# Kernel tuning notes

Measured on AMD Instinct MI355X. Metric: run time of the kernel, lower is better.

The kernel has to match this reference:

```python
import jax, jax.numpy as jnp
import numpy as np

HEADS = 4


def _dwconv(x, w, d):
    # x: (B,C,H,W), w: (C,1,3,3); reflection pad by d then dilated depthwise conv (same spatial size)
    xp = jnp.pad(x, ((0, 0), (0, 0), (d, d), (d, d)), mode='reflect')
    return jax.lax.conv_general_dilated(
        xp, w, window_strides=(1, 1), padding='VALID', rhs_dilation=(d, d),
        feature_group_count=x.shape[1], dimension_numbers=('NCHW', 'OIHW', 'NCHW'))


def _pyramid(x, w1, w2, w3):
    x0, x1, x2, x3 = jnp.split(x, 4, axis=1)
    return jnp.concatenate(
        [x0, _dwconv(x1, w1, 1), _dwconv(x2, w2, 2), _dwconv(x3, w3, 3)], axis=1)


def _conv1x1(x, w):
    return jnp.einsum('oi,bihw->bohw', w, x)


def _heads(t):
    # b (H c) h w -> b H c (h w)
    b, C, h, w = t.shape
    return t.reshape(b, HEADS, C // HEADS, h * w)


def _l2norm(t):
    # torch F.normalize(dim=-1): x / max(||x||, eps)
    return t / jnp.maximum(jnp.linalg.norm(t, axis=-1, keepdims=True), 1e-12)


def setup_inputs() -> dict:
    key = jax.random.key(0)
    ks = jax.random.split(key, 20)
    B, H, W = 2, 256, 256
    dim, dim_h, dim_l, sque = 256, 128, 64, 4
    s = 0.05
    inp = {
        'x':   jax.random.normal(ks[0], (B, dim, H, W), jnp.float32),
        'x_h': jax.random.normal(ks[1], (B, dim_h, H, W), jnp.float32),
        'x_l': jax.random.normal(ks[2], (B, dim_l, H, W), jnp.float32),
        # kv: 1x1 conv dim -> dim//sque*2 = 128, pyramid dw on 128 ch (32 per branch)
        'w_kv':  jax.random.normal(ks[3], (dim // sque * 2, dim), jnp.float32) * s,
        'kv_dw1': jax.random.normal(ks[4], (32, 1, 3, 3), jnp.float32) * s,
        'kv_dw2': jax.random.normal(ks[5], (32, 1, 3, 3), jnp.float32) * s,
        'kv_dw3': jax.random.normal(ks[6], (32, 1, 3, 3), jnp.float32) * s,
        # q_h: dim_h -> 32, pyramid branches of 8 ch
        'w_qh':  jax.random.normal(ks[7], (dim_h // sque, dim_h), jnp.float32) * s,
        'qh_dw1': jax.random.normal(ks[8], (8, 1, 3, 3), jnp.float32) * s,
        'qh_dw2': jax.random.normal(ks[9], (8, 1, 3, 3), jnp.float32) * s,
        'qh_dw3': jax.random.normal(ks[10], (8, 1, 3, 3), jnp.float32) * s,
        # q_l: dim_l -> 16, pyramid branches of 4 ch
        'w_ql':  jax.random.normal(ks[11], (dim_l // sque, dim_l), jnp.float32) * s,
        'ql_dw1': jax.random.normal(ks[12], (4, 1, 3, 3), jnp.float32) * s,
        'ql_dw2': jax.random.normal(ks[13], (4, 1, 3, 3), jnp.float32) * s,
        'ql_dw3': jax.random.normal(ks[14], (4, 1, 3, 3), jnp.float32) * s,
        'w_ph': jax.random.normal(ks[15], (dim_h, dim_h // sque), jnp.float32) * s,
        'w_pl': jax.random.normal(ks[16], (dim_l, dim_l // sque), jnp.float32) * s,
        'temperature': jnp.ones((HEADS, 1, 1), jnp.float32),
    }
    return inp


def reference(x, x_h, x_l, w_kv, kv_dw1, kv_dw2, kv_dw3,
              w_qh, qh_dw1, qh_dw2, qh_dw3,
              w_ql, ql_dw1, ql_dw2, ql_dw3,
              w_ph, w_pl, temperature):
    b, _, h, w = x.shape
    kv = _pyramid(_conv1x1(x, w_kv), kv_dw1, kv_dw2, kv_dw3)
    k, v = jnp.split(kv, 2, axis=1)
    q_h = _pyramid(_conv1x1(x_h, w_qh), qh_dw1, qh_dw2, qh_dw3)
    q_l = _pyramid(_conv1x1(x_l, w_ql), ql_dw1, ql_dw2, ql_dw3)
    k = _l2norm(_heads(k))      # (b, H, ck, N)
    v = _heads(v)               # (b, H, ck, N)
    q_h = _l2norm(_heads(q_h))  # (b, H, ch, N)
    q_l = _l2norm(_heads(q_l))  # (b, H, cl, N)
    temp = temperature[None]    # (1, H, 1, 1)

    def attend(q):
        a = jnp.einsum('bhcn,bhdn->bhcd', q, k) * temp  # channel-wise scores
        a = jax.nn.softmax(a, axis=-1)
        return jnp.einsum('bhcd,bhdn->bhcn', a, v)

    msg_h = attend(q_h).reshape(b, -1, h, w)
    msg_l = attend(q_l).reshape(b, -1, h, w)
    return _conv1x1(msg_h, w_ph), _conv1x1(msg_l, w_pl)
```

## Files before the change

### kernel.cpp

```cpp
#include <hip/hip_runtime.h>


#define NPIX 65536

using bf16x8 = __attribute__((ext_vector_type(8))) short;
using f32x4  = __attribute__((ext_vector_type(4))) float;

__device__ __forceinline__ unsigned short f2bf(float f) {
    unsigned u = __builtin_bit_cast(unsigned, f);
    u = u + 0x7FFF + ((u >> 16) & 1);
    return (unsigned short)(u >> 16);
}
__device__ __forceinline__ float bf2f(unsigned short u) {
    return __builtin_bit_cast(float, (unsigned)u << 16);
}

__global__ void zero_k(float* __restrict__ p, int n) {
    int i = blockIdx.x * 256 + threadIdx.x;
    if (i < n) p[i] = 0.f;
}

__global__ void cast_w_k(const float* __restrict__ w_kv,
                         const float* __restrict__ w_qh,
                         const float* __restrict__ w_ql,
                         unsigned short* __restrict__ wkv_b,
                         unsigned short* __restrict__ wqh_b,
                         unsigned short* __restrict__ wql_b) {
    int idx = blockIdx.x * 256 + threadIdx.x;
    if (idx < 32768) wkv_b[idx] = f2bf(w_kv[idx]);
    else if (idx < 32768 + 4096) wqh_b[idx - 32768] = f2bf(w_qh[idx - 32768]);
    else if (idx < 32768 + 4096 + 1024) wql_b[idx - 36864] = f2bf(w_ql[idx - 36864]);
}

template <int MW, int MSPLIT, int KT, bool SPLIT, bool SRCBF>
__global__ __launch_bounds__(256) void gemm_mfma_k(
    const void* __restrict__ srcv, const unsigned short* __restrict__ A,
    float* __restrict__ out, float* __restrict__ out2,
    long srcBStride, long aBStride, long outBStride, long out2BStride) {
    constexpr int K  = KT * 32;
    constexpr int RW = K / 2 + 4;
    constexpr int NW = MSPLIT;

    __shared__ unsigned Blds[64 * RW];

    const int t    = threadIdx.x;
    const int wave = t >> 6;
    const int lane = t & 63;
    const int r    = lane & 15;
    const int q    = lane >> 4;

    const int chunk = blockIdx.x;
    const int b     = chunk >> 10;
    const int n0    = (chunk & 1023) * 64;
    const int m0    = (wave % MSPLIT) * MW * 16;
    const int nb    = (wave / MSPLIT) * NW * 16;

    bf16x8 af[MW][KT];
    {
        const unsigned short* Ab = A + (size_t)b * aBStride;
#pragma unroll
        for (int mw = 0; mw < MW; ++mw)
#pragma unroll
            for (int kt = 0; kt < KT; ++kt)
                af[mw][kt] = *(const bf16x8*)(Ab + (size_t)(m0 + mw * 16 + r) * K + kt * 32 + q * 8);
    }

    {
        const int sn = t >> 2, kp0 = t & 3;
        if constexpr (SRCBF) {
            const unsigned short* sp = (const unsigned short*)srcv + (size_t)b * srcBStride + n0 + sn;
#pragma unroll
            for (int it = 0; it < K / 8; ++it) {
                const int kp = it * 4 + kp0;
                const unsigned v0 = sp[(size_t)(2 * kp) * NPIX];
                const unsigned v1 = sp[(size_t)(2 * kp + 1) * NPIX];
                Blds[sn * RW + kp] = v0 | (v1 << 16);
            }
        } else {
            const float* sp = (const float*)srcv + (size_t)b * srcBStride + n0 + sn;
#pragma unroll
            for (int it = 0; it < K / 8; ++it) {
                const int kp = it * 4 + kp0;
                const float v0 = sp[(size_t)(2 * kp) * NPIX];
                const float v1 = sp[(size_t)(2 * kp + 1) * NPIX];
                Blds[sn * RW + kp] = (unsigned)f2bf(v0) | ((unsigned)f2bf(v1) << 16);
            }
        }
    }
    __syncthreads();

    f32x4 acc[MW][NW];
#pragma unroll
    for (int mw = 0; mw < MW; ++mw)
#pragma unroll
        for (int nw = 0; nw < NW; ++nw) acc[mw][nw] = (f32x4){0.f, 0.f, 0.f, 0.f};

#pragma unroll
    for (int kt = 0; kt < KT; ++kt) {
        bf16x8 bf[NW];
#pragma unroll
        for (int nw = 0; nw < NW; ++nw) {
            const int n = nb + nw * 16 + r;
            bf[nw] = *(const bf16x8*)(&Blds[n * RW + kt * 16 + q * 4]);
        }
#pragma unroll
        for (int mw = 0; mw < MW; ++mw)
#pragma unroll
            for (int nw = 0; nw < NW; ++nw)
                acc[mw][nw] = __builtin_amdgcn_mfma_f32_16x16x32_bf16(
                    af[mw][kt], bf[nw], acc[mw][nw], 0, 0, 0);
    }

#pragma unroll
    for (int mw = 0; mw < MW; ++mw) {
        const int obase = m0 + mw * 16 + q * 4;
#pragma unroll
        for (int nw = 0; nw < NW; ++nw) {
            const int n = n0 + nb + nw * 16 + r;
#pragma unroll
            for (int rr = 0; rr < 4; ++rr) {
                const int o = obase + rr;
                float* dst;
                if (SPLIT && o >= 128)
                    dst = out2 + (size_t)b * out2BStride + (size_t)(o - 128) * NPIX + n;
                else
                    dst = out + (size_t)b * outBStride + (size_t)o * NPIX + n;
                *dst = acc[mw][nw][rr];
            }
        }
    }
}

__device__ __forceinline__ int refl(int p) {
    return (p < 0) ? -p : ((p > 255) ? 510 - p : p);
}

__global__ __launch_bounds__(256) void pyramid_k(const float* __restrict__ in,
                                                 unsigned short* __restrict__ out, int C,
                                                 const float* __restrict__ w1,
                                                 const float* __restrict__ w2,
                                                 const float* __restrict__ w3) {
    const int t = threadIdx.x;
    const int bi = blockIdx.x;
    const int y = bi & 255;
    const int bc = bi >> 8;
    const int G = C >> 2;
    const int c = bc % C;
    const int g = (c >= 3 * G) ? 3 : (c >= 2 * G) ? 2 : (c >= G) ? 1 : 0;

    const float* src = in + (size_t)bc * NPIX;
    const size_t oidx = (size_t)bc * NPIX + y * 256 + t;

    if (g == 0) {
        out[oidx] = f2bf(src[y * 256 + t]);
        return;
    }

    __shared__ float rows[3][256];
    const int y0 = refl(y - g), y2 = refl(y + g);
    for (int i = t; i < 384; i += 256) {
        const int rr  = i >> 7;
        const int off = (i & 127) * 2;
        const int yy  = (rr == 0) ? y0 : (rr == 1) ? y : y2;
        const float2 v = *(const float2*)(src + yy * 256 + off);
        rows[rr][off] = v.x;
        rows[rr][off + 1] = v.y;
    }
    __syncthreads();

    const float* wp = (g == 1 ? w1 : (g == 2 ? w2 : w3)) + (c - g * G) * 9;
    const int xm = refl(t - g), xp = refl(t + g);
    float s = 0.f;
#pragma unroll
    for (int ky = 0; ky < 3; ++ky) {
        s = fmaf(wp[ky * 3 + 0], rows[ky][xm], s);
        s = fmaf(wp[ky * 3 + 1], rows[ky][t], s);
        s = fmaf(wp[ky * 3 + 2], rows[ky][xp], s);
    }
    out[oidx] = f2bf(s);
}

__global__ __launch_bounds__(256) void scores_k(const unsigned short* __restrict__ qhp,
                                                const unsigned short* __restrict__ qlp,
                                                const unsigned short* __restrict__ kvp,
                                                float* __restrict__ Sbuf) {
    const int t = threadIdx.x;
    const int wave = t >> 6, lane = t & 63;
    const int r = lane & 15, q = lane >> 4;
    const int slice = blockIdx.x;
    const int hd = blockIdx.y;
    const int b = blockIdx.z;

    const unsigned short* qrow;
    if (r < 8)       qrow = qhp + (size_t)(b * 32 + hd * 8 + r) * NPIX;
    else if (r < 12) qrow = qlp + (size_t)(b * 16 + hd * 4 + (r - 8)) * NPIX;
    else             qrow = qhp + (size_t)(b * 32 + hd * 8) * NPIX;
    const unsigned short* krow = kvp + (size_t)(b * 128 + hd * 16 + r) * NPIX;

    const int base = slice * 1024 + wave * 256;
    f32x4 acc = (f32x4){0.f, 0.f, 0.f, 0.f};
    float qq = 0.f, kk = 0.f;
#pragma unroll
    for (int c8 = 0; c8 < 8; ++c8) {
        const int n = base + c8 * 32 + q * 8;
        const bf16x8 a  = *(const bf16x8*)(qrow + n);
        const bf16x8 bb = *(const bf16x8*)(krow + n);
        acc = __builtin_amdgcn_mfma_f32_16x16x32_bf16(a, bb, acc, 0, 0, 0);
#pragma unroll
        for (int j = 0; j < 8; ++j) {
            const float av = bf2f((unsigned short)a[j]);
            const float bv = bf2f((unsigned short)bb[j]);
            qq = fmaf(av, av, qq);
            kk = fmaf(bv, bv, kk);
        }
    }
    qq += __shfl_xor(qq, 16); qq += __shfl_xor(qq, 32);
    kk += __shfl_xor(kk, 16); kk += __shfl_xor(kk, 32);

    __shared__ float Sred[4][16][16];
    __shared__ float qred[4][16];
    __shared__ float kred[4][16];
#pragma unroll
    for (int rr = 0; rr < 4; ++rr) Sred[wave][q * 4 + rr][r] = acc[rr];
    if (q == 0) { qred[wave][r] = qq; kred[wave][r] = kk; }
    __syncthreads();

    if (t < 192) {
        const int c = t >> 4, d = t & 15;
        const float s = Sred[0][c][d] + Sred[1][c][d] + Sred[2][c][d] + Sred[3][c][d];
        if (c < 12) atomicAdd(&Sbuf[((b * 4 + hd) * 12 + c) * 16 + d], s);
    } else if (t < 208) {
        const int d = t - 192;
        const float s = kred[0][d] + kred[1][d] + kred[2][d] + kred[3][d];
        atomicAdd(&Sbuf[1536 + (b * 4 + hd) * 16 + d], s);
    } else if (t < 220) {
        const int c = t - 208;
        const float s = qred[0][c] + qred[1][c] + qred[2][c] + qred[3][c];
        atomicAdd(&Sbuf[1664 + (b * 4 + hd) * 12 + c], s);
    }
}

__global__ __launch_bounds__(256) void finalize_k(const float* __restrict__ Sbuf,
                                                  const float* __restrict__ w_ph,
                                                  const float* __restrict__ w_pl,
                                                  const float* __restrict__ temp,
                                                  unsigned short* __restrict__ CT) {
    __shared__ float As[192];
    const int t = threadIdx.x;
    const int hd = blockIdx.x;
    const int b = blockIdx.y;

    if (t < 192) {
        const int c = t >> 4, d = t & 15;
        const float kss = Sbuf[1536 + (b * 4 + hd) * 16 + d];
        const float qss = Sbuf[1664 + (b * 4 + hd) * 12 + c];
        const float invk = 1.f / fmaxf(sqrtf(kss), 1e-12f);
        const float invq = 1.f / fmaxf(sqrtf(qss), 1e-12f);
        float s = Sbuf[((b * 4 + hd) * 12 + c) * 16 + d] * invq * invk * temp[hd];
        float m = s;
        for (int mask = 8; mask >= 1; mask >>= 1) m = fmaxf(m, __shfl_xor(m, mask, 16));
        const float e = expf(s - m);
        float sum = e;
        for (int mask = 8; mask >= 1; mask >>= 1) sum += __shfl_xor(sum, mask, 16);
        As[c * 16 + d] = e / sum;
    }
    __syncthreads();

    unsigned short* CTb = CT + (size_t)b * 192 * 64;
    for (int idx = t; idx < 3072; idx += 256) {
        const int d = idx & 15, rr = idx >> 4;
        float s = 0.f;
        if (rr < 128) {
#pragma unroll
            for (int c = 0; c < 8; ++c)
                s = fmaf(w_ph[rr * 32 + hd * 8 + c], As[c * 16 + d], s);
        } else {
            const int r2 = rr - 128;
#pragma unroll
            for (int c = 0; c < 4; ++c)
                s = fmaf(w_pl[r2 * 16 + hd * 4 + c], As[(8 + c) * 16 + d], s);
        }
        CTb[(size_t)rr * 64 + hd * 16 + d] = f2bf(s);
    }
}

extern "C" void kernel_launch(void* const* d_in, const int* in_sizes, int n_in,
                              void* d_out, int out_size, void* d_ws, size_t ws_size,
                              hipStream_t stream) {
    const float* x      = (const float*)d_in[0];
    const float* x_h    = (const float*)d_in[1];
    const float* x_l    = (const float*)d_in[2];
    const float* w_kv   = (const float*)d_in[3];
    const float* kv_dw1 = (const float*)d_in[4];
    const float* kv_dw2 = (const float*)d_in[5];
    const float* kv_dw3 = (const float*)d_in[6];
    const float* w_qh   = (const float*)d_in[7];
    const float* qh_dw1 = (const float*)d_in[8];
    const float* qh_dw2 = (const float*)d_in[9];
    const float* qh_dw3 = (const float*)d_in[10];
    const float* w_ql   = (const float*)d_in[11];
    const float* ql_dw1 = (const float*)d_in[12];
    const float* ql_dw2 = (const float*)d_in[13];
    const float* ql_dw3 = (const float*)d_in[14];
    const float* w_ph   = (const float*)d_in[15];
    const float* w_pl   = (const float*)d_in[16];
    const float* temp   = (const float*)d_in[17];
    float* out = (float*)d_out;

    char* ws = (char*)d_ws;
    float*          Sbuf  = (float*)(ws + 0);
    unsigned short* wkv_b = (unsigned short*)(ws + 8192);
    unsigned short* wqh_b = (unsigned short*)(ws + 73728);
    unsigned short* wql_b = (unsigned short*)(ws + 81920);
    unsigned short* CT    = (unsigned short*)(ws + 90112);
    float*          kvraw = (float*)(ws + 262144);
    float*          qhraw = (float*)(ws + 67371008);
    float*          qlraw = (float*)(ws + 84148224);
    unsigned short* kvpyr = (unsigned short*)(ws + 92536832);
    unsigned short* qhpyr = (unsigned short*)(ws + 126091264);
    unsigned short* qlpyr = (unsigned short*)(ws + 134479872);

    zero_k<<<7, 256, 0, stream>>>(Sbuf, 1760);
    cast_w_k<<<148, 256, 0, stream>>>(w_kv, w_qh, w_ql, wkv_b, wqh_b, wql_b);

    gemm_mfma_k<2, 4, 8, false, false><<<2048, 256, 0, stream>>>(
        x, wkv_b, kvraw, nullptr, 256L * NPIX, 0L, 128L * NPIX, 0L);
    gemm_mfma_k<2, 1, 4, false, false><<<2048, 256, 0, stream>>>(
        x_h, wqh_b, qhraw, nullptr, 128L * NPIX, 0L, 32L * NPIX, 0L);
    gemm_mfma_k<1, 1, 2, false, false><<<2048, 256, 0, stream>>>(
        x_l, wql_b, qlraw, nullptr, 64L * NPIX, 0L, 16L * NPIX, 0L);

    pyramid_k<<<65536, 256, 0, stream>>>(kvraw, kvpyr, 128, kv_dw1, kv_dw2, kv_dw3);
    pyramid_k<<<16384, 256, 0, stream>>>(qhraw, qhpyr, 32, qh_dw1, qh_dw2, qh_dw3);
    pyramid_k<<<8192, 256, 0, stream>>>(qlraw, qlpyr, 16, ql_dw1, ql_dw2, ql_dw3);

    scores_k<<<dim3(64, 4, 2), 256, 0, stream>>>(qhpyr, qlpyr, kvpyr, Sbuf);
    finalize_k<<<dim3(4, 2), 256, 0, stream>>>(Sbuf, w_ph, w_pl, temp, CT);

    gemm_mfma_k<3, 4, 2, true, true><<<2048, 256, 0, stream>>>(
        (const void*)(kvpyr + 64L * NPIX), CT, out, out + 2L * 128 * NPIX,
        128L * NPIX, 192L * 64, 128L * NPIX, 64L * NPIX);
}
```

Before: 452.3 us.

## Pipeline GEMM chunks, fuse pyramid launches with row tiling, drop atomics

Each GEMM block now handles four pixel chunks, loading the next chunk from global memory into registers while computing the current one. It double-buffers an XOR-swizzled LDS tile and uses wide vector loads. The three pyramid launches become one kernel that processes 32-row tiles per plane with a shared halo, two pixels per thread and packed bf16 stores. Score reduction writes per-slice partials that finalize sums, replacing atomics and the zeroing kernel. The cost is more registers and LDS per block, fewer blocks in flight, and hand-placed waitcnt assembly that could be fragile.

```diff
diff --git a/kernel.cpp b/kernel.cpp
--- a/kernel.cpp
+++ b/kernel.cpp
@@ -5,6 +5,8 @@
 
 using bf16x8 = __attribute__((ext_vector_type(8))) short;
 using f32x4  = __attribute__((ext_vector_type(4))) float;
+using f4     = __attribute__((ext_vector_type(4))) float;
+using us4    = __attribute__((ext_vector_type(4))) unsigned short;
 
 __device__ __forceinline__ unsigned short f2bf(float f) {
     unsigned u = __builtin_bit_cast(unsigned, f);
@@ -13,11 +15,6 @@
 }
 __device__ __forceinline__ float bf2f(unsigned short u) {
     return __builtin_bit_cast(float, (unsigned)u << 16);
-}
-
-__global__ void zero_k(float* __restrict__ p, int n) {
-    int i = blockIdx.x * 256 + threadIdx.x;
-    if (i < n) p[i] = 0.f;
 }
 
 __global__ void cast_w_k(const float* __restrict__ w_kv,
@@ -32,28 +29,31 @@
     else if (idx < 32768 + 4096 + 1024) wql_b[idx - 36864] = f2bf(w_ql[idx - 36864]);
 }
 
-template <int MW, int MSPLIT, int KT, bool SPLIT, bool SRCBF>
-__global__ __launch_bounds__(256) void gemm_mfma_k(
+template <int MW, int MSPLIT, int KT, int CPB, bool SPLIT, bool SRCBF>
+__global__ __launch_bounds__(256, 2) void gemm_mfma_k(
     const void* __restrict__ srcv, const unsigned short* __restrict__ A,
     float* __restrict__ out, float* __restrict__ out2,
     long srcBStride, long aBStride, long outBStride, long out2BStride) {
-    constexpr int K  = KT * 32;
-    constexpr int RW = K / 2 + 4;
-    constexpr int NW = MSPLIT;
-
-    __shared__ unsigned Blds[64 * RW];
+    constexpr int K     = KT * 32;
+    constexpr int KW    = K / 2;
+    constexpr int NW    = MSPLIT;
+    constexpr int ITERS = K / 32;
+    constexpr int SCNT  = MW * NW * 4;
+
+    __shared__ __align__(16) unsigned Blds[2][64 * KW];
 
     const int t    = threadIdx.x;
     const int wave = t >> 6;
     const int lane = t & 63;
     const int r    = lane & 15;
     const int q    = lane >> 4;
-
-    const int chunk = blockIdx.x;
-    const int b     = chunk >> 10;
-    const int n0    = (chunk & 1023) * 64;
-    const int m0    = (wave % MSPLIT) * MW * 16;
-    const int nb    = (wave / MSPLIT) * NW * 16;
+    const int h    = t >> 4;
+    const int m4   = (t & 15) * 4;
+
+    const int chunk0 = blockIdx.x * CPB;
+    const int b      = chunk0 >> 10;
+    const int m0     = (wave % MSPLIT) * MW * 16;
+    const int nb     = (wave / MSPLIT) * NW * 16;
 
     bf16x8 af[MW][KT];
     {
@@ -65,68 +65,109 @@
                 af[mw][kt] = *(const bf16x8*)(Ab + (size_t)(m0 + mw * 16 + r) * K + kt * 32 + q * 8);
     }
 
-    {
-        const int sn = t >> 2, kp0 = t & 3;
+    f4  va[ITERS], vb[ITERS];
+    us4 ua[ITERS], ub[ITERS];
+
+    auto issue_loads = [&](int chunk) {
+        const long base = (long)(chunk & 1023) * 64 + m4;
         if constexpr (SRCBF) {
-            const unsigned short* sp = (const unsigned short*)srcv + (size_t)b * srcBStride + n0 + sn;
-#pragma unroll
-            for (int it = 0; it < K / 8; ++it) {
-                const int kp = it * 4 + kp0;
-                const unsigned v0 = sp[(size_t)(2 * kp) * NPIX];
-                const unsigned v1 = sp[(size_t)(2 * kp + 1) * NPIX];
-                Blds[sn * RW + kp] = v0 | (v1 << 16);
+            const unsigned short* sp = (const unsigned short*)srcv + (size_t)b * srcBStride + base;
+#pragma unroll
+            for (int i = 0; i < ITERS; ++i) {
+                const int kp = i * 16 + h;
+                ua[i] = *(const us4*)(sp + (size_t)(2 * kp) * NPIX);
+                ub[i] = *(const us4*)(sp + (size_t)(2 * kp + 1) * NPIX);
             }
         } else {
-            const float* sp = (const float*)srcv + (size_t)b * srcBStride + n0 + sn;
-#pragma unroll
-            for (int it = 0; it < K / 8; ++it) {
-                const int kp = it * 4 + kp0;
-                const float v0 = sp[(size_t)(2 * kp) * NPIX];
-                const float v1 = sp[(size_t)(2 * kp + 1) * NPIX];
-                Blds[sn * RW + kp] = (unsigned)f2bf(v0) | ((unsigned)f2bf(v1) << 16);
+            const float* sp = (const float*)srcv + (size_t)b * srcBStride + base;
+#pragma unroll
+            for (int i = 0; i < ITERS; ++i) {
+                const int kp = i * 16 + h;
+                va[i] = *(const f4*)(sp + (size_t)(2 * kp) * NPIX);
+                vb[i] = *(const f4*)(sp + (size_t)(2 * kp + 1) * NPIX);
             }
         }
-    }
+    };
+
+    auto write_lds = [&](unsigned* B) {
+#pragma unroll
+        for (int i = 0; i < ITERS; ++i) {
+            const int kp = i * 16 + h;
+#pragma unroll
+            for (int j = 0; j < 4; ++j) {
+                const int n = m4 + j;
+                unsigned val;
+                if constexpr (SRCBF)
+                    val = (unsigned)ua[i][j] | ((unsigned)ub[i][j] << 16);
+                else
+                    val = (unsigned)f2bf(va[i][j]) | ((unsigned)f2bf(vb[i][j]) << 16);
+                B[n * KW + ((((kp >> 2) ^ ((n >> 1) & 7)) << 2) | (kp & 3))] = val;
+            }
+        }
+    };
+
+    auto compute_chunk = [&](const unsigned* B, int n0c) {
+        f32x4 acc[MW][NW];
+#pragma unroll
+        for (int mw = 0; mw < MW; ++mw)
+#pragma unroll
+            for (int nw = 0; nw < NW; ++nw) acc[mw][nw] = (f32x4){0.f, 0.f, 0.f, 0.f};
+
+#pragma unroll
+        for (int kt = 0; kt < KT; ++kt) {
+            bf16x8 bf[NW];
+#pragma unroll
+            for (int nw = 0; nw < NW; ++nw) {
+                const int n = nb + nw * 16 + r;
+                bf[nw] = *(const bf16x8*)(&B[n * KW + (((kt * 4 + q) ^ ((n >> 1) & 7)) << 2)]);
+            }
+#pragma unroll
+            for (int mw = 0; mw < MW; ++mw)
+#pragma unroll
+                for (int nw = 0; nw < NW; ++nw)
+                    acc[mw][nw] = __builtin_amdgcn_mfma_f32_16x16x32_bf16(
+                        af[mw][kt], bf[nw], acc[mw][nw], 0, 0, 0);
+        }
+
+#pragma unroll
+        for (int mw = 0; mw < MW; ++mw) {
+            const int obase = m0 + mw * 16 + q * 4;
+#pragma unroll
+            for (int nw = 0; nw < NW; ++nw) {
+                const int n = n0c + nb + nw * 16 + r;
+#pragma unroll
+                for (int rr = 0; rr < 4; ++rr) {
+                    const int o = obase + rr;
+                    float* dst;
+                    if (SPLIT && o >= 128)
+                        dst = out2 + (size_t)b * out2BStride + (size_t)(o - 128) * NPIX + n;
+                    else
+                        dst = out + (size_t)b * outBStride + (size_t)o * NPIX + n;
+                    *dst = acc[mw][nw][rr];
+                }
+            }
+        }
+    };
+
+    issue_loads(chunk0);
+    write_lds(&Blds[0][0]);
     __syncthreads();
 
-    f32x4 acc[MW][NW];
-#pragma unroll
-    for (int mw = 0; mw < MW; ++mw)
-#pragma unroll
-        for (int nw = 0; nw < NW; ++nw) acc[mw][nw] = (f32x4){0.f, 0.f, 0.f, 0.f};
-
-#pragma unroll
-    for (int kt = 0; kt < KT; ++kt) {
-        bf16x8 bf[NW];
-#pragma unroll
-        for (int nw = 0; nw < NW; ++nw) {
-            const int n = nb + nw * 16 + r;
-            bf[nw] = *(const bf16x8*)(&Blds[n * RW + kt * 16 + q * 4]);
-        }
-#pragma unroll
-        for (int mw = 0; mw < MW; ++mw)
-#pragma unroll
-            for (int nw = 0; nw < NW; ++nw)
-                acc[mw][nw] = __builtin_amdgcn_mfma_f32_16x16x32_bf16(
-                    af[mw][kt], bf[nw], acc[mw][nw], 0, 0, 0);
-    }
-
-#pragma unroll
-    for (int mw = 0; mw < MW; ++mw) {
-        const int obase = m0 + mw * 16 + q * 4;
-#pragma unroll
-        for (int nw = 0; nw < NW; ++nw) {
-            const int n = n0 + nb + nw * 16 + r;
-#pragma unroll
-            for (int rr = 0; rr < 4; ++rr) {
-                const int o = obase + rr;
-                float* dst;
-                if (SPLIT && o >= 128)
-                    dst = out2 + (size_t)b * out2BStride + (size_t)(o - 128) * NPIX + n;
-                else
-                    dst = out + (size_t)b * outBStride + (size_t)o * NPIX + n;
-                *dst = acc[mw][nw][rr];
-            }
+#pragma unroll
+    for (int c = 0; c < CPB; ++c) {
+        if (c + 1 < CPB) {
+            issue_loads(chunk0 + c + 1);
+            __builtin_amdgcn_sched_barrier(0);
+        }
+        compute_chunk(&Blds[c & 1][0], ((chunk0 + c) & 1023) * 64);
+        if (c + 1 < CPB) {
+            asm volatile("s_waitcnt vmcnt(%0)" :: "n"(SCNT) : "memory");
+            __builtin_amdgcn_sched_barrier(0);
+            write_lds(&Blds[(c + 1) & 1][0]);
+            asm volatile("s_waitcnt lgkmcnt(0)" ::: "memory");
+            __builtin_amdgcn_sched_barrier(0);
+            __builtin_amdgcn_s_barrier();
+            __builtin_amdgcn_sched_barrier(0);
         }
     }
 }
@@ -135,55 +176,81 @@
     return (p < 0) ? -p : ((p > 255) ? 510 - p : p);
 }
 
-__global__ __launch_bounds__(256) void pyramid_k(const float* __restrict__ in,
-                                                 unsigned short* __restrict__ out, int C,
-                                                 const float* __restrict__ w1,
-                                                 const float* __restrict__ w2,
-                                                 const float* __restrict__ w3) {
-    const int t = threadIdx.x;
+__global__ __launch_bounds__(256) void pyramid_k(
+    const float* __restrict__ kvraw, const float* __restrict__ qhraw,
+    const float* __restrict__ qlraw,
+    unsigned short* __restrict__ kvp, unsigned short* __restrict__ qhp,
+    unsigned short* __restrict__ qlp,
+    const float* __restrict__ kv1, const float* __restrict__ kv2, const float* __restrict__ kv3,
+    const float* __restrict__ qh1, const float* __restrict__ qh2, const float* __restrict__ qh3,
+    const float* __restrict__ ql1, const float* __restrict__ ql2, const float* __restrict__ ql3) {
+    const int t  = threadIdx.x;
     const int bi = blockIdx.x;
-    const int y = bi & 255;
-    const int bc = bi >> 8;
+    const int yt = bi & 7, pl = bi >> 3;
+    const int y0 = yt * 32;
+
+    const float* in; unsigned short* outp; int C, c;
+    const float *w1, *w2, *w3;
+    if (pl < 256)      { in = kvraw + (size_t)pl * NPIX; outp = kvp + (size_t)pl * NPIX;
+                         C = 128; c = pl & 127; w1 = kv1; w2 = kv2; w3 = kv3; }
+    else if (pl < 320) { const int p2 = pl - 256; in = qhraw + (size_t)p2 * NPIX; outp = qhp + (size_t)p2 * NPIX;
+                         C = 32; c = p2 & 31; w1 = qh1; w2 = qh2; w3 = qh3; }
+    else               { const int p2 = pl - 320; in = qlraw + (size_t)p2 * NPIX; outp = qlp + (size_t)p2 * NPIX;
+                         C = 16; c = p2 & 15; w1 = ql1; w2 = ql2; w3 = ql3; }
     const int G = C >> 2;
-    const int c = bc % C;
     const int g = (c >= 3 * G) ? 3 : (c >= 2 * G) ? 2 : (c >= G) ? 1 : 0;
 
-    const float* src = in + (size_t)bc * NPIX;
-    const size_t oidx = (size_t)bc * NPIX + y * 256 + t;
+    const int half = t >> 7, c2 = (t & 127) * 2;
+    unsigned* outw = (unsigned*)outp;
 
     if (g == 0) {
-        out[oidx] = f2bf(src[y * 256 + t]);
+#pragma unroll
+        for (int i = 0; i < 16; ++i) {
+            const int y = y0 + half * 16 + i;
+            const float2 v = *(const float2*)(in + (size_t)y * 256 + c2);
+            outw[y * 128 + (t & 127)] = (unsigned)f2bf(v.x) | ((unsigned)f2bf(v.y) << 16);
+        }
         return;
     }
 
-    __shared__ float rows[3][256];
-    const int y0 = refl(y - g), y2 = refl(y + g);
-    for (int i = t; i < 384; i += 256) {
-        const int rr  = i >> 7;
-        const int off = (i & 127) * 2;
-        const int yy  = (rr == 0) ? y0 : (rr == 1) ? y : y2;
-        const float2 v = *(const float2*)(src + yy * 256 + off);
-        rows[rr][off] = v.x;
-        rows[rr][off + 1] = v.y;
+    __shared__ float rows[38][256];
+    for (int idx = t; idx < 38 * 64; idx += 256) {
+        const int rr2 = idx >> 6, qd = idx & 63;
+        const int yy = refl(y0 - 3 + rr2);
+        *(f4*)(&rows[rr2][qd * 4]) = *(const f4*)(in + (size_t)yy * 256 + qd * 4);
     }
     __syncthreads();
 
     const float* wp = (g == 1 ? w1 : (g == 2 ? w2 : w3)) + (c - g * G) * 9;
-    const int xm = refl(t - g), xp = refl(t + g);
-    float s = 0.f;
-#pragma unroll
-    for (int ky = 0; ky < 3; ++ky) {
-        s = fmaf(wp[ky * 3 + 0], rows[ky][xm], s);
-        s = fmaf(wp[ky * 3 + 1], rows[ky][t], s);
-        s = fmaf(wp[ky * 3 + 2], rows[ky][xp], s);
-    }
-    out[oidx] = f2bf(s);
+    float w[9];
+#pragma unroll
+    for (int i = 0; i < 9; ++i) w[i] = wp[i];
+
+    const int xm0 = refl(c2 - g), xp0 = refl(c2 + g);
+    const int xm1 = refl(c2 + 1 - g), xp1 = refl(c2 + 1 + g);
+
+#pragma unroll
+    for (int i = 0; i < 16; ++i) {
+        const int ro = half * 16 + i;
+        float s0 = 0.f, s1 = 0.f;
+#pragma unroll
+        for (int ky = 0; ky < 3; ++ky) {
+            const float* rp = rows[ro + 3 + (ky - 1) * g];
+            s0 = fmaf(w[ky * 3 + 0], rp[xm0], s0);
+            s0 = fmaf(w[ky * 3 + 1], rp[c2], s0);
+            s0 = fmaf(w[ky * 3 + 2], rp[xp0], s0);
+            s1 = fmaf(w[ky * 3 + 0], rp[xm1], s1);
+            s1 = fmaf(w[ky * 3 + 1], rp[c2 + 1], s1);
+            s1 = fmaf(w[ky * 3 + 2], rp[xp1], s1);
+        }
+        outw[(y0 + ro) * 128 + (t & 127)] = (unsigned)f2bf(s0) | ((unsigned)f2bf(s1) << 16);
+    }
 }
 
 __global__ __launch_bounds__(256) void scores_k(const unsigned short* __restrict__ qhp,
                                                 const unsigned short* __restrict__ qlp,
                                                 const unsigned short* __restrict__ kvp,
-                                                float* __restrict__ Sbuf) {
+                                                float* __restrict__ part) {
     const int t = threadIdx.x;
     const int wave = t >> 6, lane = t & 63;
     const int r = lane & 15, q = lane >> 4;
@@ -225,38 +292,44 @@
     if (q == 0) { qred[wave][r] = qq; kred[wave][r] = kk; }
     __syncthreads();
 
+    float* pb = part + ((size_t)((b * 4 + hd) * 64 + slice)) * 224;
     if (t < 192) {
         const int c = t >> 4, d = t & 15;
-        const float s = Sred[0][c][d] + Sred[1][c][d] + Sred[2][c][d] + Sred[3][c][d];
-        if (c < 12) atomicAdd(&Sbuf[((b * 4 + hd) * 12 + c) * 16 + d], s);
+        pb[t] = Sred[0][c][d] + Sred[1][c][d] + Sred[2][c][d] + Sred[3][c][d];
     } else if (t < 208) {
         const int d = t - 192;
-        const float s = kred[0][d] + kred[1][d] + kred[2][d] + kred[3][d];
-        atomicAdd(&Sbuf[1536 + (b * 4 + hd) * 16 + d], s);
+        pb[t] = kred[0][d] + kred[1][d] + kred[2][d] + kred[3][d];
     } else if (t < 220) {
         const int c = t - 208;
-        const float s = qred[0][c] + qred[1][c] + qred[2][c] + qred[3][c];
-        atomicAdd(&Sbuf[1664 + (b * 4 + hd) * 12 + c], s);
-    }
-}
-
-__global__ __launch_bounds__(256) void finalize_k(const float* __restrict__ Sbuf,
+        pb[t] = qred[0][c] + qred[1][c] + qred[2][c] + qred[3][c];
+    }
+}
+
+__global__ __launch_bounds__(256) void finalize_k(const float* __restrict__ part,
                                                   const float* __restrict__ w_ph,
                                                   const float* __restrict__ w_pl,
                                                   const float* __restrict__ temp,
                                                   unsigned short* __restrict__ CT) {
     __shared__ float As[192];
+    __shared__ float kks[16];
+    __shared__ float qqs[12];
     const int t = threadIdx.x;
     const int hd = blockIdx.x;
     const int b = blockIdx.y;
 
+    const float* pb = part + ((size_t)(b * 4 + hd) * 64) * 224;
+    float acc = 0.f;
+    if (t < 220)
+        for (int s2 = 0; s2 < 64; ++s2) acc += pb[s2 * 224 + t];
+    if (t >= 192 && t < 208) kks[t - 192] = acc;
+    else if (t >= 208 && t < 220) qqs[t - 208] = acc;
+    __syncthreads();
+
     if (t < 192) {
         const int c = t >> 4, d = t & 15;
-        const float kss = Sbuf[1536 + (b * 4 + hd) * 16 + d];
-        const float qss = Sbuf[1664 + (b * 4 + hd) * 12 + c];
-        const float invk = 1.f / fmaxf(sqrtf(kss), 1e-12f);
-        const float invq = 1.f / fmaxf(sqrtf(qss), 1e-12f);
-        float s = Sbuf[((b * 4 + hd) * 12 + c) * 16 + d] * invq * invk * temp[hd];
+        const float invk = 1.f / fmaxf(sqrtf(kks[d]), 1e-12f);
+        const float invq = 1.f / fmaxf(sqrtf(qqs[c]), 1e-12f);
+        float s = acc * invq * invk * temp[hd];
         float m = s;
         for (int mask = 8; mask >= 1; mask >>= 1) m = fmaxf(m, __shfl_xor(m, mask, 16));
         const float e = expf(s - m);
@@ -308,36 +381,36 @@
     float* out = (float*)d_out;
 
     char* ws = (char*)d_ws;
-    float*          Sbuf  = (float*)(ws + 0);
-    unsigned short* wkv_b = (unsigned short*)(ws + 8192);
-    unsigned short* wqh_b = (unsigned short*)(ws + 73728);
-    unsigned short* wql_b = (unsigned short*)(ws + 81920);
-    unsigned short* CT    = (unsigned short*)(ws + 90112);
-    float*          kvraw = (float*)(ws + 262144);
-    float*          qhraw = (float*)(ws + 67371008);
-    float*          qlraw = (float*)(ws + 84148224);
-    unsigned short* kvpyr = (unsigned short*)(ws + 92536832);
-    unsigned short* qhpyr = (unsigned short*)(ws + 126091264);
-    unsigned short* qlpyr = (unsigned short*)(ws + 134479872);
-
-    zero_k<<<7, 256, 0, stream>>>(Sbuf, 1760);
+    float*          part  = (float*)(ws + 0);
+    unsigned short* wkv_b = (unsigned short*)(ws + 458752);
+    unsigned short* wqh_b = (unsigned short*)(ws + 524288);
+    unsigned short* wql_b = (unsigned short*)(ws + 532480);
+    unsigned short* CT    = (unsigned short*)(ws + 540672);
+    float*          kvraw = (float*)(ws + 589824);
+    float*          qhraw = (float*)(ws + 67698688);
+    float*          qlraw = (float*)(ws + 84475904);
+    unsigned short* kvpyr = (unsigned short*)(ws + 92864512);
+    unsigned short* qhpyr = (unsigned short*)(ws + 126418944);
+    unsigned short* qlpyr = (unsigned short*)(ws + 134807552);
+
     cast_w_k<<<148, 256, 0, stream>>>(w_kv, w_qh, w_ql, wkv_b, wqh_b, wql_b);
 
-    gemm_mfma_k<2, 4, 8, false, false><<<2048, 256, 0, stream>>>(
+    gemm_mfma_k<2, 4, 8, 4, false, false><<<512, 256, 0, stream>>>(
         x, wkv_b, kvraw, nullptr, 256L * NPIX, 0L, 128L * NPIX, 0L);
-    gemm_mfma_k<2, 1, 4, false, false><<<2048, 256, 0, stream>>>(
+    gemm_mfma_k<2, 1, 4, 4, false, false><<<512, 256, 0, stream>>>(
         x_h, wqh_b, qhraw, nullptr, 128L * NPIX, 0L, 32L * NPIX, 0L);
-    gemm_mfma_k<1, 1, 2, false, false><<<2048, 256, 0, stream>>>(
+    gemm_mfma_k<1, 1, 2, 4, false, false><<<512, 256, 0, stream>>>(
         x_l, wql_b, qlraw, nullptr, 64L * NPIX, 0L, 16L * NPIX, 0L);
 
-    pyramid_k<<<65536, 256, 0, stream>>>(kvraw, kvpyr, 128, kv_dw1, kv_dw2, kv_dw3);
-    pyramid_k<<<16384, 256, 0, stream>>>(qhraw, qhpyr, 32, qh_dw1, qh_dw2, qh_dw3);
-    pyramid_k<<<8192, 256, 0, stream>>>(qlraw, qlpyr, 16, ql_dw1, ql_dw2, ql_dw3);
-
-    scores_k<<<dim3(64, 4, 2), 256, 0, stream>>>(qhpyr, qlpyr, kvpyr, Sbuf);
-    finalize_k<<<dim3(4, 2), 256, 0, stream>>>(Sbuf, w_ph, w_pl, temp, CT);
-
-    gemm_mfma_k<3, 4, 2, true, true><<<2048, 256, 0, stream>>>(
+    pyramid_k<<<2816, 256, 0, stream>>>(kvraw, qhraw, qlraw, kvpyr, qhpyr, qlpyr,
+                                        kv_dw1, kv_dw2, kv_dw3,
+                                        qh_dw1, qh_dw2, qh_dw3,
+                                        ql_dw1, ql_dw2, ql_dw3);
+
+    scores_k<<<dim3(64, 4, 2), 256, 0, stream>>>(qhpyr, qlpyr, kvpyr, part);
+    finalize_k<<<dim3(4, 2), 256, 0, stream>>>(part, w_ph, w_pl, temp, CT);
+
+    gemm_mfma_k<3, 4, 2, 4, true, true><<<512, 256, 0, stream>>>(
         (const void*)(kvpyr + 64L * NPIX), CT, out, out + 2L * 128 * NPIX,
         128L * NPIX, 192L * 64, 128L * NPIX, 64L * NPIX);
 }
```

Result: faster. 400.0 us (-11.6%).
